# Kernel optimization log

Hardware: AMD Instinct MI355X
Metric: run time of the kernel (lower is better)

Reference implementation:

```python
import jax, jax.numpy as jnp
import numpy as np

N_USERS = 100000
N_ITEMS = 200000
N = N_USERS + N_ITEMS
D = 64
NNZ = 4_000_000
N_HOPS = 3
EDGE_DROP = 0.5   # keep prob (torch.floor(rate + u) keeps with prob=rate)
MESS_DROP = 0.1
EPS_PERT = 0.03
LN_EPS = 1e-5


def setup_inputs() -> dict:
    key = jax.random.key(0)
    k1, k2, k3, k4 = jax.random.split(key, 4)
    user_embed = jax.random.normal(k1, (N_USERS, D), dtype=jnp.float32) * 0.1
    item_embed = jax.random.normal(k2, (N_ITEMS, D), dtype=jnp.float32) * 0.1
    adj_indices = jax.random.randint(k3, (2, NNZ), 0, N, dtype=jnp.int32)
    adj_values = jax.random.uniform(k4, (NNZ,), dtype=jnp.float32)
    gamma = jnp.ones((D,), dtype=jnp.float32)
    beta = jnp.zeros((D,), dtype=jnp.float32)
    return {"user_embed": user_embed, "item_embed": item_embed,
            "adj_values": adj_values, "gamma": gamma, "beta": beta,
            "adj_indices": adj_indices}


def _layer_norm(x, g, b):
    mu = jnp.mean(x, axis=-1, keepdims=True)
    var = jnp.mean(jnp.square(x - mu), axis=-1, keepdims=True)
    return (x - mu) * jax.lax.rsqrt(var + LN_EPS) * g + b


def reference(user_embed, item_embed, adj_values, gamma, beta, adj_indices):
    rows, cols = adj_indices[0], adj_indices[1]
    all_embed = jnp.concatenate([user_embed, item_embed], axis=0)  # [N, D]
    agg = all_embed
    embs = [all_embed]
    rng = jax.random.key(42)
    for hop in range(N_HOPS):
        kh = jax.random.fold_in(rng, hop)
        ke, km, kp = jax.random.split(kh, 3)
        # sparse edge dropout: floor(rate + U(0,1)) -> keep with prob=rate, rescale 1/(1-rate)
        edge_mask = jnp.floor(EDGE_DROP + jax.random.uniform(ke, (NNZ,)))
        vals = adj_values * edge_mask * (1.0 / (1.0 - EDGE_DROP))
        # spmm: out[r] += v * agg[c] for each edge (r, c)
        msg = vals[:, None] * jnp.take(agg, cols, axis=0)            # [NNZ, D]
        agg = jax.ops.segment_sum(msg, rows, num_segments=N)         # [N, D]
        agg = _layer_norm(agg, gamma, beta)
        # message dropout (nn.Dropout): drop with prob p, scale 1/(1-p)
        keep = (jax.random.uniform(km, agg.shape) >= MESS_DROP).astype(agg.dtype)
        agg = agg * keep * (1.0 / (1.0 - MESS_DROP))
        # sign-scaled noise perturbation (F.normalize along dim=-1)
        noise = jax.random.normal(kp, agg.shape, dtype=agg.dtype)
        noise = noise / (jnp.linalg.norm(noise, axis=-1, keepdims=True) + 1e-12)
        agg = agg + jnp.sign(agg) * noise * EPS_PERT
        embs.append(agg)
    embs = jnp.stack(embs, axis=1)  # [N, n_hops+1, D]
    cl = embs[:, 1, :]              # agg after hop 0
    return (embs[:N_USERS], embs[N_USERS:], cl[:N_USERS], cl[N_USERS:])
```

## Files before the change

kernel.cpp:

```cpp
#include <hip/hip_runtime.h>
#include <stdint.h>

#define N_USERS 100000
#define N_ITEMS 200000
#define NTOT    300000
#define DIM     64
#define NNZ     4000000

#define OUT_I    25600000
#define OUT_CLU  76800000
#define OUT_CLI  83200000

#define COLMASK  0x7FFFFu

#define RPB   1024
#define NB    ((NTOT + RPB - 1) / RPB)
#define TILE  4096
#define BCAP  20480
#define HCAP  2500000

typedef float floatx4 __attribute__((ext_vector_type(4)));
typedef uint32_t u32x4 __attribute__((ext_vector_type(4)));
typedef unsigned short ushortx4 __attribute__((ext_vector_type(4)));

__host__ __device__ __forceinline__ void tf2x32(uint32_t k0, uint32_t k1,
                                                uint32_t x0, uint32_t x1,
                                                uint32_t& o0, uint32_t& o1) {
  uint32_t ks2 = k0 ^ k1 ^ 0x1BD11BDAu;
#define TFR(r) { x0 += x1; x1 = (x1 << (r)) | (x1 >> (32 - (r))); x1 ^= x0; }
  x0 += k0; x1 += k1;
  TFR(13) TFR(15) TFR(26) TFR(6)
  x0 += k1;  x1 += ks2 + 1u;
  TFR(17) TFR(29) TFR(16) TFR(24)
  x0 += ks2; x1 += k0 + 2u;
  TFR(13) TFR(15) TFR(26) TFR(6)
  x0 += k0;  x1 += k1 + 3u;
  TFR(17) TFR(29) TFR(16) TFR(24)
  x0 += k1;  x1 += ks2 + 4u;
  TFR(13) TFR(15) TFR(26) TFR(6)
  x0 += ks2; x1 += k0 + 5u;
#undef TFR
  o0 = x0; o1 = x1;
}

__device__ __forceinline__ uint32_t rnd_bits(uint32_t k0, uint32_t k1, uint32_t j) {
  uint32_t a, b;
  tf2x32(k0, k1, 0u, j, a, b);
  return a ^ b;
}

__device__ __forceinline__ float u01f(uint32_t bits) {
  return __uint_as_float((bits >> 9) | 0x3f800000u) - 1.0f;
}

__device__ __forceinline__ unsigned short f2bf(float f) {
  uint32_t u = __float_as_uint(f);
  return (unsigned short)((u + 0x7FFFu + ((u >> 16) & 1u)) >> 16);
}

__device__ __forceinline__ float erfinv_giles(float x) {
  float w = -__logf((1.0f - x) * (1.0f + x));
  float wc = w - 2.5f;
  float p1 = 2.81022636e-08f;
  p1 = fmaf(p1, wc, 3.43273939e-07f);
  p1 = fmaf(p1, wc, -3.5233877e-06f);
  p1 = fmaf(p1, wc, -4.39150654e-06f);
  p1 = fmaf(p1, wc, 0.00021858087f);
  p1 = fmaf(p1, wc, -0.00125372503f);
  p1 = fmaf(p1, wc, -0.00417768164f);
  p1 = fmaf(p1, wc, 0.246640727f);
  p1 = fmaf(p1, wc, 1.50140941f);
  float wt = __builtin_sqrtf(w) - 3.0f;
  float p2 = -0.000200214257f;
  p2 = fmaf(p2, wt, 0.000100950558f);
  p2 = fmaf(p2, wt, 0.00134934322f);
  p2 = fmaf(p2, wt, -0.00367342844f);
  p2 = fmaf(p2, wt, 0.00573950773f);
  p2 = fmaf(p2, wt, -0.0076224613f);
  p2 = fmaf(p2, wt, 0.00943887047f);
  p2 = fmaf(p2, wt, 1.00167406f);
  p2 = fmaf(p2, wt, 2.83297682f);
  float p = (w < 5.0f) ? p1 : p2;
  return p * x;
}

__device__ __forceinline__ void sload_se(const int2* p, int& s, int& e) {
  uint64_t r;
  asm volatile("s_load_dwordx2 %0, %1, 0x0\n\t"
               "s_waitcnt lgkmcnt(0)"
               : "=&s"(r) : "s"(p));
  s = (int)(uint32_t)r;
  e = (int)(uint32_t)(r >> 32);
}
__device__ __forceinline__ void sload_rec8(const uint2* p, u32x4& a, u32x4& b,
                                           u32x4& c, u32x4& d) {
  asm volatile("s_load_dwordx4 %0, %4, 0x0\n\t"
               "s_load_dwordx4 %1, %4, 0x10\n\t"
               "s_load_dwordx4 %2, %4, 0x20\n\t"
               "s_load_dwordx4 %3, %4, 0x30\n\t"
               "s_waitcnt lgkmcnt(0)"
               : "=&s"(a), "=&s"(b), "=&s"(c), "=&s"(d) : "s"(p));
}
__device__ __forceinline__ void sload_rec2(const uint2* p, u32x4& a) {
  asm volatile("s_load_dwordx4 %0, %1, 0x0\n\t"
               "s_waitcnt lgkmcnt(0)"
               : "=&s"(a) : "s"(p));
}

__global__ __launch_bounds__(256) void k_bin(const int* __restrict__ rows,
                                             const int* __restrict__ cols,
                                             const float* __restrict__ adjv,
                                             int* __restrict__ gcount,
                                             uint2* __restrict__ staging,
                                             uint32_t ke00, uint32_t ke01,
                                             uint32_t ke10, uint32_t ke11,
                                             uint32_t ke20, uint32_t ke21, int nnz) {
  __shared__ int hist[NB];
  __shared__ int gb[NB];
  int t = threadIdx.x;
  for (int i = t; i < NB; i += 256) hist[i] = 0;
  __syncthreads();
  int base = blockIdx.x * TILE;

  uint32_t recx[16];
  float    recy[16];
  uint32_t bl[16];

#pragma unroll
  for (int i = 0; i < 16; i++) {
    int e = base + i * 256 + t;
    bl[i] = 0xFFFFFFFFu;
    if (e < nnz) {
      int r = rows[e];
      uint32_t c = (uint32_t)cols[e];
      uint32_t m0 = rnd_bits(ke00, ke01, (uint32_t)e) >> 31;
      uint32_t m1 = rnd_bits(ke10, ke11, (uint32_t)e) >> 31;
      uint32_t m2 = rnd_bits(ke20, ke21, (uint32_t)e) >> 31;
      recx[i] = c | (m0 << 19) | (m1 << 20) | (m2 << 21) | ((uint32_t)(r & (RPB - 1)) << 22);
      recy[i] = adjv[e] * 2.0f;
      int b = r >> 10;
      int lp = atomicAdd(&hist[b], 1);
      bl[i] = ((uint32_t)b << 13) | (uint32_t)lp;
    }
  }
  __syncthreads();
  for (int i = t; i < NB; i += 256) {
    int c = hist[i];
    gb[i] = c ? atomicAdd(&gcount[i], c) : 0;
  }
  __syncthreads();
#pragma unroll
  for (int i = 0; i < 16; i++) {
    if (bl[i] != 0xFFFFFFFFu) {
      int b  = (int)(bl[i] >> 13);
      int lp = (int)(bl[i] & 0x1FFFu);
      staging[(size_t)b * BCAP + gb[b] + lp] = make_uint2(recx[i], __float_as_uint(recy[i]));
    }
  }
}

__global__ __launch_bounds__(256) void k_place3(const int* __restrict__ gcount,
                                                const uint2* __restrict__ staging,
                                                uint2* __restrict__ packed3,
                                                int2* __restrict__ rowse3,
                                                int* __restrict__ gtail) {
  __shared__ int cnt[3][RPB];
  __shared__ int off[3][RPB];
  __shared__ int sm[256];
  __shared__ int gbh[3];
  int b = blockIdx.x;
  int t = threadIdx.x;
  int r0 = b << 10;
  for (int j = t; j < RPB; j += 256) { cnt[0][j] = 0; cnt[1][j] = 0; cnt[2][j] = 0; }
  __syncthreads();
  int ln = gcount[b];
  const uint2* run = staging + (size_t)b * BCAP;

  for (int i = t; i < ln; i += 256) {
    uint32_t w = run[i].x;
    int rl = (int)(w >> 22);
    if (w & (1u << 19)) atomicAdd(&cnt[0][rl], 1);
    if (w & (1u << 20)) atomicAdd(&cnt[1][rl], 1);
    if (w & (1u << 21)) atomicAdd(&cnt[2][rl], 1);
  }
  __syncthreads();

  for (int h = 0; h < 3; h++) {
    int j0 = t * 4;
    int c0 = cnt[h][j0], c1 = cnt[h][j0 + 1], c2 = cnt[h][j0 + 2], c3 = cnt[h][j0 + 3];
    int e0 = (c0 + 1) & ~1, e1 = (c1 + 1) & ~1, e2 = (c2 + 1) & ~1, e3 = (c3 + 1) & ~1;
    int s4 = e0 + e1 + e2 + e3;
    sm[t] = s4;
    __syncthreads();
    for (int o2 = 1; o2 < 256; o2 <<= 1) {
      int y = (t >= o2) ? sm[t - o2] : 0;
      __syncthreads();
      sm[t] += y;
      __syncthreads();
    }
    int ex = sm[t] - s4;
    off[h][j0]     = ex;
    off[h][j0 + 1] = ex + e0;
    off[h][j0 + 2] = ex + e0 + e1;
    off[h][j0 + 3] = ex + e0 + e1 + e2;
    if (t == 255) gbh[h] = atomicAdd(&gtail[h], sm[255]);
    __syncthreads();
  }

  int nr = min(RPB, NTOT - r0);
  for (int h = 0; h < 3; h++) {
    int gb = gbh[h];
    for (int j = t; j < RPB; j += 256) {
      int raw = cnt[h][j];
      int start = gb + off[h][j];
      off[h][j] = start;
      if (j < nr) {
        rowse3[h * NTOT + r0 + j] = make_int2(start, start + ((raw + 1) & ~1));
        if (raw & 1) packed3[(size_t)h * HCAP + start + raw] = make_uint2(0u, 0u);
      }
    }
  }
  __syncthreads();

  for (int i = t; i < ln; i += 256) {
    uint2 rec = run[i];
    int rl = (int)(rec.x >> 22);
    uint2 orec = make_uint2(rec.x & COLMASK, rec.y);
    if (rec.x & (1u << 19)) { int p = atomicAdd(&off[0][rl], 1); packed3[0 * (size_t)HCAP + p] = orec; }
    if (rec.x & (1u << 20)) { int p = atomicAdd(&off[1][rl], 1); packed3[1 * (size_t)HCAP + p] = orec; }
    if (rec.x & (1u << 21)) { int p = atomicAdd(&off[2][rl], 1); packed3[2 * (size_t)HCAP + p] = orec; }
  }
}

__global__ void k_init0(const float* __restrict__ ue, const float* __restrict__ ie,
                        float* __restrict__ out, unsigned short* __restrict__ T0) {
  int t = blockIdx.x * blockDim.x + threadIdx.x;
  if (t >= NTOT * DIM / 4) return;
  int j = t * 4;
  int r = j >> 6;
  int d = j & 63;
  floatx4 v = (r < N_USERS) ? *reinterpret_cast<const floatx4*>(ue + j)
                            : *reinterpret_cast<const floatx4*>(ie + (j - N_USERS * DIM));
  int o = (r < N_USERS) ? (r * 256 + d) : (OUT_I + (r - N_USERS) * 256 + d);
  __builtin_nontemporal_store(v, reinterpret_cast<floatx4*>(out + o));
  ushortx4 bv;
  bv.x = f2bf(v.x); bv.y = f2bf(v.y); bv.z = f2bf(v.z); bv.w = f2bf(v.w);
  *reinterpret_cast<ushortx4*>(T0 + j) = bv;
}

template <int HOP>
__global__ __launch_bounds__(256) void k_hop(const int2* __restrict__ rowse,
                                             const uint2* __restrict__ packed,
                                             const unsigned short* __restrict__ Tin,
                                             unsigned short* __restrict__ Tout,
                                             const float* __restrict__ gamma,
                                             const float* __restrict__ beta,
                                             float* __restrict__ out,
                                             uint32_t km0, uint32_t km1,
                                             uint32_t kp0, uint32_t kp1) {
  int lane = threadIdx.x & 63;
  int r = __builtin_amdgcn_readfirstlane((int)(blockIdx.x * blockDim.x + threadIdx.x) >> 6);
  if (r >= NTOT) return;
  int s, e;
  sload_se(rowse + r, s, e);
  s = max(s, 0);
  e = min(e, HCAP);

#define GA(c, vbits, a) {                                                       \
    float xv = __uint_as_float((uint32_t)Tin[(c) * DIM + lane] << 16);          \
    a = fmaf(__uint_as_float(vbits), xv, a); }
  float acc0 = 0.0f, acc1 = 0.0f, acc2 = 0.0f, acc3 = 0.0f;
  int k = s;
  for (; k + 7 < e; k += 8) {
    u32x4 qa, qb, qc, qd;
    sload_rec8(packed + k, qa, qb, qc, qd);
    GA(qa.x, qa.y, acc0) GA(qa.z, qa.w, acc1)
    GA(qb.x, qb.y, acc2) GA(qb.z, qb.w, acc3)
    GA(qc.x, qc.y, acc0) GA(qc.z, qc.w, acc1)
    GA(qd.x, qd.y, acc2) GA(qd.z, qd.w, acc3)
  }
  for (; k + 1 < e; k += 2) {
    u32x4 qa;
    sload_rec2(packed + k, qa);
    GA(qa.x, qa.y, acc0) GA(qa.z, qa.w, acc1)
  }
#undef GA

  float x = (acc0 + acc1) + (acc2 + acc3);

  float s1 = x, s2 = x * x;
#pragma unroll
  for (int mm = 32; mm >= 1; mm >>= 1) {
    s1 += __shfl_xor(s1, mm, 64);
    s2 += __shfl_xor(s2, mm, 64);
  }
  float mu = s1 * (1.0f / 64.0f);
  float var = fmaxf(s2 * (1.0f / 64.0f) - mu * mu, 0.0f);
  x = (x - mu) * rsqrtf(var + 1e-5f) * gamma[lane] + beta[lane];

  uint32_t j = (uint32_t)(r * DIM + lane);
  float um = u01f(rnd_bits(km0, km1, j));
  const float INV_KEEP = (float)(1.0 / 0.9);
  x = x * ((um >= 0.1f) ? INV_KEEP : 0.0f);

  float un = u01f(rnd_bits(kp0, kp1, j));
  const float LO = __uint_as_float(0xBF7FFFFFu);
  float val = un * 2.0f + LO;
  float nz = 0x1.6a09e6p+0f * erfinv_giles(val);
  float q2 = nz * nz;
#pragma unroll
  for (int mm = 32; mm >= 1; mm >>= 1) q2 += __shfl_xor(q2, mm, 64);
  float nrm = __builtin_sqrtf(q2);
  float nh = nz / (nrm + 1e-12f);
  float sg = (x > 0.0f) ? 1.0f : ((x < 0.0f) ? -1.0f : 0.0f);
  x = x + sg * nh * 0.03f;

  if (HOP < 2) Tout[r * DIM + lane] = f2bf(x);
  constexpr int h1 = HOP + 1;
  if (r < N_USERS) {
    __builtin_nontemporal_store(x, &out[r * 256 + h1 * 64 + lane]);
    if (HOP == 0) __builtin_nontemporal_store(x, &out[OUT_CLU + r * 64 + lane]);
  } else {
    int i = r - N_USERS;
    __builtin_nontemporal_store(x, &out[OUT_I + i * 256 + h1 * 64 + lane]);
    if (HOP == 0) __builtin_nontemporal_store(x, &out[OUT_CLI + i * 64 + lane]);
  }
}

extern "C" void kernel_launch(void* const* d_in, const int* in_sizes, int n_in,
                              void* d_out, int out_size, void* d_ws, size_t ws_size,
                              hipStream_t stream) {
  (void)in_sizes; (void)n_in; (void)out_size; (void)ws_size;
  const float* ue    = (const float*)d_in[0];
  const float* ie    = (const float*)d_in[1];
  const float* adjv  = (const float*)d_in[2];
  const float* gamma = (const float*)d_in[3];
  const float* beta  = (const float*)d_in[4];
  const int*   adji  = (const int*)d_in[5];
  const int* rows = adji;
  const int* cols = adji + NNZ;
  float* out = (float*)d_out;

  char* ws = (char*)d_ws;
  size_t off = 0;
  auto alloc = [&](size_t bytes) -> void* {
    void* p = ws + off;
    off += (bytes + 255) & ~(size_t)255;
    return p;
  };
  unsigned short* TA = (unsigned short*)alloc(sizeof(short) * NTOT * DIM);
  unsigned short* TB = (unsigned short*)alloc(sizeof(short) * NTOT * DIM);
  int*   gcount  = (int*)alloc(sizeof(int) * NB);
  int*   gtail   = (int*)alloc(sizeof(int) * 4);
  int2*  rowse3  = (int2*)alloc(sizeof(int2) * 3 * NTOT);
  uint2* staging = (uint2*)alloc(sizeof(uint2) * (size_t)NB * BCAP);
  uint2* packed3 = (uint2*)alloc(sizeof(uint2) * 3 * (size_t)HCAP);

  uint32_t K[3][6];
  for (uint32_t h = 0; h < 3; h++) {
    uint32_t h0, h1;
    tf2x32(0u, 42u, 0u, h, h0, h1);
    tf2x32(h0, h1, 0u, 0u, K[h][0], K[h][1]);
    tf2x32(h0, h1, 0u, 1u, K[h][2], K[h][3]);
    tf2x32(h0, h1, 0u, 2u, K[h][4], K[h][5]);
  }

  const int nbT = (NNZ + TILE - 1) / TILE;
  (void)hipMemsetAsync(gcount, 0, sizeof(int) * NB, stream);
  (void)hipMemsetAsync(gtail, 0, sizeof(int) * 4, stream);

  k_bin<<<nbT, 256, 0, stream>>>(rows, cols, adjv, gcount, staging,
                                 K[0][0], K[0][1], K[1][0], K[1][1],
                                 K[2][0], K[2][1], NNZ);
  k_place3<<<NB, 256, 0, stream>>>(gcount, staging, packed3, rowse3, gtail);
  k_init0<<<(NTOT * DIM / 4 + 255) / 256, 256, 0, stream>>>(ue, ie, out, TA);

  const int nbH = (NTOT * DIM + 255) / 256;
  k_hop<0><<<nbH, 256, 0, stream>>>(rowse3 + 0 * NTOT, packed3 + 0 * (size_t)HCAP,
                                    TA, TB, gamma, beta, out,
                                    K[0][2], K[0][3], K[0][4], K[0][5]);
  k_hop<1><<<nbH, 256, 0, stream>>>(rowse3 + 1 * NTOT, packed3 + 1 * (size_t)HCAP,
                                    TB, TA, gamma, beta, out,
                                    K[1][2], K[1][3], K[1][4], K[1][5]);
  k_hop<2><<<nbH, 256, 0, stream>>>(rowse3 + 2 * NTOT, packed3 + 2 * (size_t)HCAP,
                                    TA, nullptr, gamma, beta, out,
                                    K[2][2], K[2][3], K[2][4], K[2][5]);
}
```

Baseline: 643.7 us.

## Merge init into bin kernel and gather two edges per wave with dword loads

```diff
diff --git a/kernel.cpp b/kernel.cpp
--- a/kernel.cpp
+++ b/kernel.cpp
@@ -16,6 +16,7 @@
 #define RPB   1024
 #define NB    ((NTOT + RPB - 1) / RPB)
 #define TILE  4096
+#define NBT   ((NNZ + TILE - 1) / TILE)
 #define BCAP  20480
 #define HCAP  2500000
 
@@ -101,22 +102,54 @@
                "s_waitcnt lgkmcnt(0)"
                : "=&s"(a), "=&s"(b), "=&s"(c), "=&s"(d) : "s"(p));
 }
+__device__ __forceinline__ void sload_rec6(const uint2* p, u32x4& a, u32x4& b, u32x4& c) {
+  asm volatile("s_load_dwordx4 %0, %3, 0x0\n\t"
+               "s_load_dwordx4 %1, %3, 0x10\n\t"
+               "s_load_dwordx4 %2, %3, 0x20\n\t"
+               "s_waitcnt lgkmcnt(0)"
+               : "=&s"(a), "=&s"(b), "=&s"(c) : "s"(p));
+}
+__device__ __forceinline__ void sload_rec4(const uint2* p, u32x4& a, u32x4& b) {
+  asm volatile("s_load_dwordx4 %0, %2, 0x0\n\t"
+               "s_load_dwordx4 %1, %2, 0x10\n\t"
+               "s_waitcnt lgkmcnt(0)"
+               : "=&s"(a), "=&s"(b) : "s"(p));
+}
 __device__ __forceinline__ void sload_rec2(const uint2* p, u32x4& a) {
   asm volatile("s_load_dwordx4 %0, %1, 0x0\n\t"
                "s_waitcnt lgkmcnt(0)"
                : "=&s"(a) : "s"(p));
 }
 
-__global__ __launch_bounds__(256) void k_bin(const int* __restrict__ rows,
-                                             const int* __restrict__ cols,
-                                             const float* __restrict__ adjv,
-                                             int* __restrict__ gcount,
-                                             uint2* __restrict__ staging,
-                                             uint32_t ke00, uint32_t ke01,
-                                             uint32_t ke10, uint32_t ke11,
-                                             uint32_t ke20, uint32_t ke21, int nnz) {
+__global__ __launch_bounds__(256) void k_bin_init(const int* __restrict__ rows,
+                                                  const int* __restrict__ cols,
+                                                  const float* __restrict__ adjv,
+                                                  int* __restrict__ gcount,
+                                                  uint2* __restrict__ staging,
+                                                  const float* __restrict__ ue,
+                                                  const float* __restrict__ ie,
+                                                  float* __restrict__ out,
+                                                  unsigned short* __restrict__ T0,
+                                                  uint32_t ke00, uint32_t ke01,
+                                                  uint32_t ke10, uint32_t ke11,
+                                                  uint32_t ke20, uint32_t ke21) {
   __shared__ int hist[NB];
   __shared__ int gb[NB];
+  if (blockIdx.x >= NBT) {
+    int t = (blockIdx.x - NBT) * 256 + threadIdx.x;
+    if (t >= NTOT * DIM / 4) return;
+    int j = t * 4;
+    int r = j >> 6;
+    int d = j & 63;
+    floatx4 v = (r < N_USERS) ? *reinterpret_cast<const floatx4*>(ue + j)
+                              : *reinterpret_cast<const floatx4*>(ie + (j - N_USERS * DIM));
+    int o = (r < N_USERS) ? (r * 256 + d) : (OUT_I + (r - N_USERS) * 256 + d);
+    __builtin_nontemporal_store(v, reinterpret_cast<floatx4*>(out + o));
+    ushortx4 bv;
+    bv.x = f2bf(v.x); bv.y = f2bf(v.y); bv.z = f2bf(v.z); bv.w = f2bf(v.w);
+    *reinterpret_cast<ushortx4*>(T0 + j) = bv;
+    return;
+  }
   int t = threadIdx.x;
   for (int i = t; i < NB; i += 256) hist[i] = 0;
   __syncthreads();
@@ -130,7 +163,7 @@
   for (int i = 0; i < 16; i++) {
     int e = base + i * 256 + t;
     bl[i] = 0xFFFFFFFFu;
-    if (e < nnz) {
+    if (e < NNZ) {
       int r = rows[e];
       uint32_t c = (uint32_t)cols[e];
       uint32_t m0 = rnd_bits(ke00, ke01, (uint32_t)e) >> 31;
@@ -232,22 +265,6 @@
   }
 }
 
-__global__ void k_init0(const float* __restrict__ ue, const float* __restrict__ ie,
-                        float* __restrict__ out, unsigned short* __restrict__ T0) {
-  int t = blockIdx.x * blockDim.x + threadIdx.x;
-  if (t >= NTOT * DIM / 4) return;
-  int j = t * 4;
-  int r = j >> 6;
-  int d = j & 63;
-  floatx4 v = (r < N_USERS) ? *reinterpret_cast<const floatx4*>(ue + j)
-                            : *reinterpret_cast<const floatx4*>(ie + (j - N_USERS * DIM));
-  int o = (r < N_USERS) ? (r * 256 + d) : (OUT_I + (r - N_USERS) * 256 + d);
-  __builtin_nontemporal_store(v, reinterpret_cast<floatx4*>(out + o));
-  ushortx4 bv;
-  bv.x = f2bf(v.x); bv.y = f2bf(v.y); bv.z = f2bf(v.z); bv.w = f2bf(v.w);
-  *reinterpret_cast<ushortx4*>(T0 + j) = bv;
-}
-
 template <int HOP>
 __global__ __launch_bounds__(256) void k_hop(const int2* __restrict__ rowse,
                                              const uint2* __restrict__ packed,
@@ -259,34 +276,48 @@
                                              uint32_t km0, uint32_t km1,
                                              uint32_t kp0, uint32_t kp1) {
   int lane = threadIdx.x & 63;
+  bool hi = lane >= 32;
+  int l31 = lane & 31;
   int r = __builtin_amdgcn_readfirstlane((int)(blockIdx.x * blockDim.x + threadIdx.x) >> 6);
   if (r >= NTOT) return;
   int s, e;
   sload_se(rowse + r, s, e);
   s = max(s, 0);
   e = min(e, HCAP);
-
-#define GA(c, vbits, a) {                                                       \
-    float xv = __uint_as_float((uint32_t)Tin[(c) * DIM + lane] << 16);          \
-    a = fmaf(__uint_as_float(vbits), xv, a); }
-  float acc0 = 0.0f, acc1 = 0.0f, acc2 = 0.0f, acc3 = 0.0f;
+  const uint32_t* __restrict__ T32 = (const uint32_t*)Tin;
+
+#define PAIR(q, alo, ahi) {                                                     \
+    uint32_t cc = hi ? (uint32_t)q.z : (uint32_t)q.x;                           \
+    uint32_t vv = hi ? (uint32_t)q.w : (uint32_t)q.y;                           \
+    uint32_t u = T32[cc * 32 + l31];                                            \
+    float vf = __uint_as_float(vv);                                             \
+    alo = fmaf(vf, __uint_as_float(u << 16), alo);                              \
+    ahi = fmaf(vf, __uint_as_float(u & 0xFFFF0000u), ahi); }
+
+  float lo0 = 0.0f, hi0 = 0.0f, lo1 = 0.0f, hi1 = 0.0f;
   int k = s;
   for (; k + 7 < e; k += 8) {
     u32x4 qa, qb, qc, qd;
     sload_rec8(packed + k, qa, qb, qc, qd);
-    GA(qa.x, qa.y, acc0) GA(qa.z, qa.w, acc1)
-    GA(qb.x, qb.y, acc2) GA(qb.z, qb.w, acc3)
-    GA(qc.x, qc.y, acc0) GA(qc.z, qc.w, acc1)
-    GA(qd.x, qd.y, acc2) GA(qd.z, qd.w, acc3)
-  }
-  for (; k + 1 < e; k += 2) {
-    u32x4 qa;
-    sload_rec2(packed + k, qa);
-    GA(qa.x, qa.y, acc0) GA(qa.z, qa.w, acc1)
-  }
-#undef GA
-
-  float x = (acc0 + acc1) + (acc2 + acc3);
+    PAIR(qa, lo0, hi0) PAIR(qb, lo1, hi1)
+    PAIR(qc, lo0, hi0) PAIR(qd, lo1, hi1)
+  }
+  {
+    int rem = e - k;
+    u32x4 qa, qb, qc;
+    if (rem == 6) { sload_rec6(packed + k, qa, qb, qc); PAIR(qa, lo0, hi0) PAIR(qb, lo1, hi1) PAIR(qc, lo0, hi0) }
+    else if (rem == 4) { sload_rec4(packed + k, qa, qb); PAIR(qa, lo0, hi0) PAIR(qb, lo1, hi1) }
+    else if (rem == 2) { sload_rec2(packed + k, qa); PAIR(qa, lo0, hi0) }
+  }
+#undef PAIR
+
+  float alo = lo0 + lo1;
+  float ahi = hi0 + hi1;
+  alo += __shfl_xor(alo, 32, 64);
+  ahi += __shfl_xor(ahi, 32, 64);
+  float xlo = __shfl(alo, lane >> 1, 64);
+  float xhi = __shfl(ahi, lane >> 1, 64);
+  float x = (lane & 1) ? xhi : xlo;
 
   float s1 = x, s2 = x * x;
 #pragma unroll
@@ -365,15 +396,15 @@
     tf2x32(h0, h1, 0u, 2u, K[h][4], K[h][5]);
   }
 
-  const int nbT = (NNZ + TILE - 1) / TILE;
   (void)hipMemsetAsync(gcount, 0, sizeof(int) * NB, stream);
   (void)hipMemsetAsync(gtail, 0, sizeof(int) * 4, stream);
 
-  k_bin<<<nbT, 256, 0, stream>>>(rows, cols, adjv, gcount, staging,
-                                 K[0][0], K[0][1], K[1][0], K[1][1],
-                                 K[2][0], K[2][1], NNZ);
+  const int nbInit = (NTOT * DIM / 4 + 255) / 256;
+  k_bin_init<<<NBT + nbInit, 256, 0, stream>>>(rows, cols, adjv, gcount, staging,
+                                               ue, ie, out, TA,
+                                               K[0][0], K[0][1], K[1][0], K[1][1],
+                                               K[2][0], K[2][1]);
   k_place3<<<NB, 256, 0, stream>>>(gcount, staging, packed3, rowse3, gtail);
-  k_init0<<<(NTOT * DIM / 4 + 255) / 256, 256, 0, stream>>>(ue, ie, out, TA);
 
   const int nbH = (NTOT * DIM + 255) / 256;
   k_hop<0><<<nbH, 256, 0, stream>>>(rowse3 + 0 * NTOT, packed3 + 0 * (size_t)HCAP,
```

Result: faster. 616.7 us (median of 2 runs) (-4.2%).
